# Kernel optimization log

Measured on AMD Instinct MI355X. Metric: run time of the kernel, lower is better.

The kernel has to match this reference:

```python
import jax, jax.numpy as jnp
import numpy as np

EMBED = 1024
HEADS = 16
HEAD_DIM = EMBED // HEADS

def setup_inputs() -> dict:
    key = jax.random.key(0)
    ks = jax.random.split(key, 12)
    N, L, E = 4, 2048, EMBED
    s = 1.0 / np.sqrt(E)
    return {
        "values": jax.random.normal(ks[0], (N, L, E), jnp.float32),
        "keys": jax.random.normal(ks[1], (N, L, E), jnp.float32),
        "query": jax.random.normal(ks[2], (N, L, E), jnp.float32),
        "mask": jnp.ones((N, 1, 1, L), jnp.int32),
        "Wv": jax.random.normal(ks[3], (E, E), jnp.float32) * s,
        "bv": jnp.zeros((E,), jnp.float32),
        "Wk": jax.random.normal(ks[4], (E, E), jnp.float32) * s,
        "bk": jnp.zeros((E,), jnp.float32),
        "Wq": jax.random.normal(ks[5], (E, E), jnp.float32) * s,
        "bq": jnp.zeros((E,), jnp.float32),
        "Wo": jax.random.normal(ks[6], (E, E), jnp.float32) * s,
        "bo": jnp.zeros((E,), jnp.float32),
    }

def reference(values, keys, query, mask, Wv, bv, Wk, bk, Wq, bq, Wo, bo):
    N, L, E = values.shape
    H, D = HEADS, HEAD_DIM
    v = (values @ Wv + bv).reshape(N, L, H, D)
    k = (keys @ Wk + bk).reshape(N, L, H, D)
    q = (query @ Wq + bq).reshape(N, L, H, D)
    # energy: [N, H, Lq, Lk]
    energy = jnp.einsum('nqhd,nkhd->nhqk', q, k)
    energy = jnp.where(mask == 0, jnp.float32(-1e20), energy)
    attn = jax.nn.softmax(energy / np.sqrt(D), axis=3)
    out = jnp.einsum('nhqk,nkhd->nqhd', attn, v).reshape(N, L, E)
    return out @ Wo + bo
```

## Files before the change

kernel.cpp:

```cpp
#include <hip/hip_runtime.h>
#include <hip/hip_bf16.h>


#define N_B 4
#define L_S 2048
#define E_D 1024
#define H_N 16
#define D_H 64

typedef __attribute__((ext_vector_type(8))) short short8;
typedef __attribute__((ext_vector_type(8))) unsigned short ushort8;
typedef __attribute__((ext_vector_type(4))) unsigned short ushort4v;
typedef __attribute__((ext_vector_type(4))) float f32x4;

#define EXP2F(x) __builtin_amdgcn_exp2f(x)

__device__ __forceinline__ unsigned short f2b(float f) {
    unsigned int u = __builtin_bit_cast(unsigned int, f);
    u += 0x7fffu + ((u >> 16) & 1u);
    return (unsigned short)(u >> 16);
}

__device__ __forceinline__ void gload16(const void* g, void* l) {
    __builtin_amdgcn_global_load_lds(
        (const __attribute__((address_space(1))) void*)g,
        (__attribute__((address_space(3))) void*)l, 16, 0, 0);
}

__global__ __launch_bounds__(256) void cvt3_kernel(const float* __restrict__ v,
                                                   const float* __restrict__ k,
                                                   const float* __restrict__ q,
                                                   unsigned short* __restrict__ out) {
    int z = blockIdx.y;
    const float* in = (z == 0) ? v : ((z == 1) ? k : q);
    unsigned short* o = out + (size_t)z * (8u << 20);
    size_t i = (size_t)blockIdx.x * 256 + threadIdx.x;
    const float* p = in + i * 8;
    ushort8 ov;
#pragma unroll
    for (int j = 0; j < 8; j++) ov[j] = f2b(p[j]);
    *(ushort8*)(o + i * 8) = ov;
}

__global__ __launch_bounds__(256) void wtrans4_kernel(const float* __restrict__ W0,
                                                      const float* __restrict__ W1,
                                                      const float* __restrict__ W2,
                                                      const float* __restrict__ W3,
                                                      unsigned short* __restrict__ WtBase) {
    __shared__ float t[64][65];
    int z = blockIdx.z;
    const float* W = (z == 0) ? W0 : ((z == 1) ? W1 : ((z == 2) ? W2 : W3));
    unsigned short* Wt = WtBase + (size_t)z * (1u << 20);
    int bx = blockIdx.x, by = blockIdx.y;
    int tx = threadIdx.x;
    int r0 = tx >> 4;
    int c4 = (tx & 15) << 2;
#pragma unroll
    for (int rr = 0; rr < 64; rr += 16) {
        const float* src = W + (size_t)(by * 64 + rr + r0) * E_D + bx * 64 + c4;
        float4 v = *(const float4*)src;
        t[rr + r0][c4 + 0] = v.x; t[rr + r0][c4 + 1] = v.y;
        t[rr + r0][c4 + 2] = v.z; t[rr + r0][c4 + 3] = v.w;
    }
    __syncthreads();
#pragma unroll
    for (int rr = 0; rr < 64; rr += 16) {
        int nrow = bx * 64 + rr + r0;
        ushort4v o;
#pragma unroll
        for (int j = 0; j < 4; j++) o[j] = f2b(t[c4 + j][rr + r0]);
        *(ushort4v*)(Wt + (size_t)nrow * E_D + by * 64 + c4) = o;
    }
}

template <int OUTMODE>
__device__ __forceinline__ void gemm_body(
    const unsigned short* __restrict__ A, const unsigned short* __restrict__ Bt,
    const float* __restrict__ bias, void* __restrict__ C,
    int K, int Nc, float scale,
    unsigned short* As, unsigned short* Bs, int n0, int m0) {
    int lane = threadIdx.x & 63, wave = threadIdx.x >> 6;
    int wr = (wave >> 1) * 64, wc = (wave & 1) * 64;
    f32x4 acc[4][4] = {};
    int nk = K >> 6;
    for (int kt = 0; kt < nk; ++kt) {
#pragma unroll
        for (int i = 0; i < 4; i++) {
            int c = (i * 4 + wave) * 64 + lane;
            int row = c >> 3;
            int csw = (c & 7) ^ (row & 7);
            gload16(A + (size_t)(m0 + row) * K + kt * 64 + csw * 8,
                    As + (size_t)(i * 4 + wave) * 512);
            gload16(Bt + (size_t)(n0 + row) * K + kt * 64 + csw * 8,
                    Bs + (size_t)(i * 4 + wave) * 512);
        }
        __syncthreads();
#pragma unroll
        for (int ks = 0; ks < 2; ++ks) {
            short8 a[4], b[4];
#pragma unroll
            for (int mi = 0; mi < 4; mi++) {
                int row = wr + mi * 16 + (lane & 15);
                int ch = (ks * 4 + (lane >> 4)) ^ (row & 7);
                a[mi] = *(const short8*)(As + row * 64 + ch * 8);
            }
#pragma unroll
            for (int ni = 0; ni < 4; ni++) {
                int col = wc + ni * 16 + (lane & 15);
                int ch = (ks * 4 + (lane >> 4)) ^ (col & 7);
                b[ni] = *(const short8*)(Bs + col * 64 + ch * 8);
            }
#pragma unroll
            for (int mi = 0; mi < 4; mi++)
#pragma unroll
                for (int ni = 0; ni < 4; ni++)
                    acc[mi][ni] = __builtin_amdgcn_mfma_f32_16x16x32_bf16(
                        a[mi], b[ni], acc[mi][ni], 0, 0, 0);
        }
        __syncthreads();
    }
    if (OUTMODE == 2) {
        int g = lane >> 4, c = lane & 15;
        unsigned short* tb = As + wave * 4096;
#pragma unroll
        for (int ni = 0; ni < 4; ni++) {
            int cl = ni * 16 + c;
            float bb = bias[n0 + wc + cl];
#pragma unroll
            for (int mi = 0; mi < 4; mi++) {
#pragma unroll
                for (int r = 0; r < 4; r++) {
                    int rl = mi * 16 + g * 4 + r;
                    tb[rl * 64 + (((cl >> 3) ^ (rl & 7)) << 3) + (cl & 7)] =
                        f2b((acc[mi][ni][r] + bb) * scale);
                }
            }
        }
        int mrow = m0 + wr;
        int n = mrow >> 11;
        int l0 = mrow & 2047;
        int h = (n0 + wc) >> 6;
        unsigned short* vt = (unsigned short*)C;
#pragma unroll
        for (int i = 0; i < 8; i++) {
            int d = i * 8 + (lane >> 3);
            int lc = (lane & 7) * 8;
            ushort8 ov;
#pragma unroll
            for (int j = 0; j < 8; j++) {
                int rl = lc + j;
                ov[j] = tb[rl * 64 + (((d >> 3) ^ (rl & 7)) << 3) + (d & 7)];
            }
            *(ushort8*)(vt + (size_t)((n * H_N + h) * D_H + d) * L_S + l0 + lc) = ov;
        }
        return;
    }
#pragma unroll
    for (int ni = 0; ni < 4; ni++) {
        int col = n0 + wc + ni * 16 + (lane & 15);
        float bb = bias[col];
#pragma unroll
        for (int mi = 0; mi < 4; mi++) {
            int rbase = m0 + wr + mi * 16 + (lane >> 4) * 4;
#pragma unroll
            for (int r = 0; r < 4; r++) {
                float v = (acc[mi][ni][r] + bb) * scale;
                if (OUTMODE == 1)
                    ((float*)C)[(size_t)(rbase + r) * Nc + col] = v;
                else
                    ((unsigned short*)C)[(size_t)(rbase + r) * Nc + col] = f2b(v);
            }
        }
    }
}

template <int OUTMODE>
__global__ __launch_bounds__(256, 2) void gemm_kernel(
    const unsigned short* __restrict__ A, const unsigned short* __restrict__ Bt,
    const float* __restrict__ bias, void* __restrict__ C,
    int M, int K, int Nc, float scale) {
    __shared__ unsigned short SMEM[2][128 * 64];
    gemm_body<OUTMODE>(A, Bt, bias, C, K, Nc, scale, SMEM[0], SMEM[1],
                       blockIdx.x * 128, blockIdx.y * 128);
}

__global__ __launch_bounds__(256, 2) void gemm3_kernel(
    const unsigned short* __restrict__ Abase, const unsigned short* __restrict__ Wtbase,
    const float* __restrict__ bv, const float* __restrict__ bk, const float* __restrict__ bq,
    unsigned short* __restrict__ vT, unsigned short* __restrict__ kbf,
    unsigned short* __restrict__ qbf, float qscale) {
    __shared__ unsigned short SMEM[2][128 * 64];
    int z = blockIdx.z;
    const unsigned short* A  = Abase + (size_t)z * (8u << 20);
    const unsigned short* Bt = Wtbase + (size_t)z * (1u << 20);
    int n0 = blockIdx.x * 128, m0 = blockIdx.y * 128;
    if (z == 0) {
        gemm_body<2>(A, Bt, bv, vT, E_D, E_D, 1.0f, SMEM[0], SMEM[1], n0, m0);
    } else if (z == 1) {
        gemm_body<0>(A, Bt, bk, kbf, E_D, E_D, 1.0f, SMEM[0], SMEM[1], n0, m0);
    } else {
        gemm_body<0>(A, Bt, bq, qbf, E_D, E_D, qscale, SMEM[0], SMEM[1], n0, m0);
    }
}

__global__ __launch_bounds__(512, 4) void attn_kernel(
    const unsigned short* __restrict__ qb, const unsigned short* __restrict__ kb,
    const unsigned short* __restrict__ vt, const int* __restrict__ mask,
    unsigned short* __restrict__ aout) {
    __shared__ unsigned short Ks[2][64 * 64];
    __shared__ unsigned short Vs[2][64 * 64];
    __shared__ unsigned short Ps[8][32 * 64];
    __shared__ alignas(8) unsigned char okb[256];
    int lane = threadIdx.x & 63, wave = threadIdx.x >> 6;
    int g = lane >> 4, c = lane & 15;
    const float SHIFT = 20.0f;

    int bid = blockIdx.x;
    int xcd = bid & 7, idx = bid >> 3;
    int grp = xcd * 8 + (idx >> 3);
    int q0 = (idx & 7) * 256;
    int h = grp & 15;
    int n = grp >> 4;

    const unsigned short* qptr  = qb + (size_t)n * L_S * E_D + h * 64;
    const unsigned short* kbase = kb + (size_t)n * L_S * E_D + h * 64;
    const unsigned short* vbase = vt + (size_t)(n * H_N + h) * D_H * L_S;
    const int* mbase = mask + n * L_S;

    if (threadIdx.x < 256) {
        int t8 = threadIdx.x * 8;
        int4 ma = *(const int4*)(mbase + t8);
        int4 mb = *(const int4*)(mbase + t8 + 4);
        int ok = (ma.x != 0) & (ma.y != 0) & (ma.z != 0) & (ma.w != 0) &
                 (mb.x != 0) & (mb.y != 0) & (mb.z != 0) & (mb.w != 0);
        okb[threadIdx.x] = (unsigned char)ok;
    }
    unsigned short* Qs = &Ps[0][0];
#pragma unroll
    for (int i = 0; i < 4; i++) {
        int ci = i * 8 + wave;
        int cc = ci * 64 + lane;
        int row = cc >> 3, csw = (cc & 7) ^ (row & 7);
        gload16(qptr + (size_t)(q0 + row) * E_D + csw * 8, Qs + (size_t)ci * 512);
    }
    {
        int cc = wave * 64 + lane;
        int row = cc >> 3, csw = (cc & 7) ^ (row & 7);
        gload16(kbase + (size_t)row * E_D + csw * 8, Ks[0] + wave * 512);
        gload16(vbase + (size_t)row * L_S + csw * 8, Vs[0] + wave * 512);
    }
    __syncthreads();

    short8 qf[2][2];
#pragma unroll
    for (int m = 0; m < 2; m++)
#pragma unroll
        for (int kd = 0; kd < 2; kd++) {
            int row = wave * 32 + m * 16 + c;
            int ch = (kd * 4 + g) ^ (row & 7);
            qf[m][kd] = *(const short8*)(Qs + row * 64 + ch * 8);
        }

    f32x4 o[2][4] = {};
    float lrun[2] = {0.f, 0.f};
    unsigned short* pw = &Ps[wave][0];

    const int NT = L_S / 64;
    for (int kt = 0; kt < NT; ++kt) {
        int cur = kt & 1;
        if (kt + 1 < NT) {
            int cc = wave * 64 + lane;
            int row = cc >> 3, csw = (cc & 7) ^ (row & 7);
            gload16(kbase + (size_t)((kt + 1) * 64 + row) * E_D + csw * 8,
                    Ks[cur ^ 1] + wave * 512);
            gload16(vbase + (size_t)row * L_S + (kt + 1) * 64 + csw * 8,
                    Vs[cur ^ 1] + wave * 512);
            asm volatile("s_waitcnt vmcnt(2)" ::: "memory");
        } else {
            asm volatile("s_waitcnt vmcnt(0)" ::: "memory");
        }
        __builtin_amdgcn_s_barrier();
        __builtin_amdgcn_sched_barrier(0);

        const unsigned short* KsC = Ks[cur];
        const unsigned short* VsC = Vs[cur];

        f32x4 sT[2][4] = {};
        __builtin_amdgcn_s_setprio(1);
#pragma unroll
        for (int kd = 0; kd < 2; kd++)
#pragma unroll
            for (int kg = 0; kg < 4; kg++) {
                int krow = kg * 16 + c;
                int ch = (kd * 4 + g) ^ (krow & 7);
                short8 kf = *(const short8*)(KsC + krow * 64 + ch * 8);
                sT[0][kg] = __builtin_amdgcn_mfma_f32_16x16x32_bf16(kf, qf[0][kd], sT[0][kg], 0, 0, 0);
                sT[1][kg] = __builtin_amdgcn_mfma_f32_16x16x32_bf16(kf, qf[1][kd], sT[1][kg], 0, 0, 0);
            }
        __builtin_amdgcn_s_setprio(0);

        uint2 fl = *(const uint2*)&okb[kt * 8];
        bool dense = ((fl.x & fl.y) == 0x01010101u);
        if (!dense) {
#pragma unroll
            for (int kg = 0; kg < 4; kg++) {
                int4 mv = *(const int4*)(mbase + kt * 64 + kg * 16 + g * 4);
                float m0 = mv.x ? 0.f : -1e30f;
                float m1 = mv.y ? 0.f : -1e30f;
                float m2 = mv.z ? 0.f : -1e30f;
                float m3 = mv.w ? 0.f : -1e30f;
                sT[0][kg][0] += m0; sT[1][kg][0] += m0;
                sT[0][kg][1] += m1; sT[1][kg][1] += m1;
                sT[0][kg][2] += m2; sT[1][kg][2] += m2;
                sT[0][kg][3] += m3; sT[1][kg][3] += m3;
            }
        }
#pragma unroll
        for (int m = 0; m < 2; m++) {
            float ps = 0.f;
            int prow = m * 16 + c;
#pragma unroll
            for (int kg = 0; kg < 4; kg++) {
                float p0 = EXP2F(sT[m][kg][0] - SHIFT);
                float p1 = EXP2F(sT[m][kg][1] - SHIFT);
                float p2 = EXP2F(sT[m][kg][2] - SHIFT);
                float p3 = EXP2F(sT[m][kg][3] - SHIFT);
                ps += (p0 + p1) + (p2 + p3);
                unsigned int w0, w1;
                asm("v_cvt_pk_bf16_f32 %0, %1, %2" : "=v"(w0) : "v"(p0), "v"(p1));
                asm("v_cvt_pk_bf16_f32 %0, %1, %2" : "=v"(w1) : "v"(p2), "v"(p3));
                int c16 = kg * 2 + (g >> 1);
                int off = prow * 64 + ((c16 ^ (prow & 7)) << 3) + ((g & 1) << 2);
                uint2 wv; wv.x = w0; wv.y = w1;
                *(uint2*)(pw + off) = wv;
            }
            ps += __shfl_xor(ps, 16);
            ps += __shfl_xor(ps, 32);
            lrun[m] += ps;
        }
        __builtin_amdgcn_s_setprio(1);
#pragma unroll
        for (int kk = 0; kk < 2; kk++) {
            short8 pb[2];
#pragma unroll
            for (int m = 0; m < 2; m++) {
                int prow = m * 16 + c;
                int ch = (kk * 4 + g) ^ (prow & 7);
                pb[m] = *(const short8*)(pw + prow * 64 + ch * 8);
            }
#pragma unroll
            for (int dg = 0; dg < 4; dg++) {
                int drow = dg * 16 + c;
                int ch = (kk * 4 + g) ^ (drow & 7);
                short8 vb = *(const short8*)(VsC + drow * 64 + ch * 8);
                o[0][dg] = __builtin_amdgcn_mfma_f32_16x16x32_bf16(vb, pb[0], o[0][dg], 0, 0, 0);
                o[1][dg] = __builtin_amdgcn_mfma_f32_16x16x32_bf16(vb, pb[1], o[1][dg], 0, 0, 0);
            }
        }
        __builtin_amdgcn_s_setprio(0);
        asm volatile("s_waitcnt lgkmcnt(0)" ::: "memory");
        __builtin_amdgcn_s_barrier();
    }
#pragma unroll
    for (int m = 0; m < 2; m++) {
        float inv = 1.f / lrun[m];
        int row = q0 + wave * 32 + m * 16 + c;
#pragma unroll
        for (int dg = 0; dg < 4; dg++) {
            ushort4v ov;
#pragma unroll
            for (int r = 0; r < 4; r++) ov[r] = f2b(o[m][dg][r] * inv);
            *(ushort4v*)(aout + (size_t)(n * L_S + row) * E_D + h * 64 + dg * 16 + g * 4) = ov;
        }
    }
}

extern "C" void kernel_launch(void* const* d_in, const int* in_sizes, int n_in,
                              void* d_out, int out_size, void* d_ws, size_t ws_size,
                              hipStream_t stream) {
    const float* values = (const float*)d_in[0];
    const float* keys   = (const float*)d_in[1];
    const float* query  = (const float*)d_in[2];
    const int*   mask   = (const int*)d_in[3];
    const float* Wv = (const float*)d_in[4];  const float* bv = (const float*)d_in[5];
    const float* Wk = (const float*)d_in[6];  const float* bk = (const float*)d_in[7];
    const float* Wq = (const float*)d_in[8];  const float* bq = (const float*)d_in[9];
    const float* Wo = (const float*)d_in[10]; const float* bo = (const float*)d_in[11];
    float* out = (float*)d_out;
    char* ws = (char*)d_ws;
    const size_t MB = 1ull << 20;
    unsigned short* xv  = (unsigned short*)(ws + 0 * MB);
    unsigned short* wtv = (unsigned short*)(ws + 48 * MB);
    unsigned short* wto = (unsigned short*)(ws + 54 * MB);
    unsigned short* vT  = (unsigned short*)(ws + 56 * MB);
    unsigned short* kbf = (unsigned short*)(ws + 72 * MB);
    unsigned short* qbf = (unsigned short*)(ws + 88 * MB);
    unsigned short* aob = (unsigned short*)(ws + 16 * MB);

    const float QS = 0.125f * 1.4426950408889634f;

    cvt3_kernel<<<dim3(4096, 3), 256, 0, stream>>>(values, keys, query, xv);
    wtrans4_kernel<<<dim3(16, 16, 4), 256, 0, stream>>>(Wv, Wk, Wq, Wo, wtv);
    gemm3_kernel<<<dim3(E_D / 128, (N_B * L_S) / 128, 3), 256, 0, stream>>>(
        xv, wtv, bv, bk, bq, vT, kbf, qbf, QS);
    attn_kernel<<<dim3(512), 512, 0, stream>>>(qbf, kbf, vT, mask, aob);
    gemm_kernel<1><<<dim3(E_D / 128, (N_B * L_S) / 128), 256, 0, stream>>>(
        aob, wto, bo, out, N_B * L_S, E_D, E_D, 1.0f);
}
```

Before: 212.1 us.

## Switch attention to 32x32x16 MFMA and keep P in registers

Rewrites the attention kernel's inner loop to use 32x32x16 bf16 MFMA tiles instead of 16x16x32. The probability tile is now built in registers with a cross-half-wave shuffle rather than written to and read back from per-wave LDS. This removes the Ps shared buffer, which shrinks LDS use and could allow higher occupancy, and it cuts LDS traffic. In exchange it adds lane shuffles, and the output stores become scalar 2-byte writes instead of vectorized ones.

```diff
diff --git a/kernel.cpp b/kernel.cpp
--- a/kernel.cpp
+++ b/kernel.cpp
@@ -12,6 +12,8 @@
 typedef __attribute__((ext_vector_type(8))) unsigned short ushort8;
 typedef __attribute__((ext_vector_type(4))) unsigned short ushort4v;
 typedef __attribute__((ext_vector_type(4))) float f32x4;
+typedef __attribute__((ext_vector_type(16))) float f32x16;
+typedef __attribute__((ext_vector_type(4))) unsigned int uint4v;
 
 #define EXP2F(x) __builtin_amdgcn_exp2f(x)
 
@@ -25,6 +27,12 @@
     __builtin_amdgcn_global_load_lds(
         (const __attribute__((address_space(1))) void*)g,
         (__attribute__((address_space(3))) void*)l, 16, 0, 0);
+}
+
+__device__ __forceinline__ unsigned int cvtpk(float a, float b) {
+    unsigned int w;
+    asm("v_cvt_pk_bf16_f32 %0, %1, %2" : "=v"(w) : "v"(a), "v"(b));
+    return w;
 }
 
 __global__ __launch_bounds__(256) void cvt3_kernel(const float* __restrict__ v,
@@ -207,24 +215,22 @@
     const unsigned short* __restrict__ qb, const unsigned short* __restrict__ kb,
     const unsigned short* __restrict__ vt, const int* __restrict__ mask,
     unsigned short* __restrict__ aout) {
-    __shared__ unsigned short Ks[2][64 * 64];
-    __shared__ unsigned short Vs[2][64 * 64];
-    __shared__ unsigned short Ps[8][32 * 64];
+    __shared__ unsigned short KV[4][64 * 64];
     __shared__ alignas(8) unsigned char okb[256];
     int lane = threadIdx.x & 63, wave = threadIdx.x >> 6;
-    int g = lane >> 4, c = lane & 15;
+    int qc = lane & 31, hl = lane >> 5;
     const float SHIFT = 20.0f;
 
     int bid = blockIdx.x;
     int xcd = bid & 7, idx = bid >> 3;
     int grp = xcd * 8 + (idx >> 3);
     int q0 = (idx & 7) * 256;
-    int h = grp & 15;
+    int hd = grp & 15;
     int n = grp >> 4;
 
-    const unsigned short* qptr  = qb + (size_t)n * L_S * E_D + h * 64;
-    const unsigned short* kbase = kb + (size_t)n * L_S * E_D + h * 64;
-    const unsigned short* vbase = vt + (size_t)(n * H_N + h) * D_H * L_S;
+    const unsigned short* qptr  = qb + (size_t)n * L_S * E_D + hd * 64;
+    const unsigned short* kbase = kb + (size_t)n * L_S * E_D + hd * 64;
+    const unsigned short* vbase = vt + (size_t)(n * H_N + hd) * D_H * L_S;
     const int* mbase = mask + n * L_S;
 
     if (threadIdx.x < 256) {
@@ -235,7 +241,7 @@
                  (mb.x != 0) & (mb.y != 0) & (mb.z != 0) & (mb.w != 0);
         okb[threadIdx.x] = (unsigned char)ok;
     }
-    unsigned short* Qs = &Ps[0][0];
+    unsigned short* Qs = &KV[0][0];
 #pragma unroll
     for (int i = 0; i < 4; i++) {
         int ci = i * 8 + wave;
@@ -243,27 +249,25 @@
         int row = cc >> 3, csw = (cc & 7) ^ (row & 7);
         gload16(qptr + (size_t)(q0 + row) * E_D + csw * 8, Qs + (size_t)ci * 512);
     }
+    __syncthreads();
+    short8 qf[4];
+#pragma unroll
+    for (int dk = 0; dk < 4; dk++) {
+        int row = wave * 32 + qc;
+        int ch = (dk * 2 + hl) ^ (row & 7);
+        qf[dk] = *(const short8*)(Qs + row * 64 + ch * 8);
+    }
+    asm volatile("s_waitcnt lgkmcnt(0)" ::: "memory");
+    __syncthreads();
     {
         int cc = wave * 64 + lane;
         int row = cc >> 3, csw = (cc & 7) ^ (row & 7);
-        gload16(kbase + (size_t)row * E_D + csw * 8, Ks[0] + wave * 512);
-        gload16(vbase + (size_t)row * L_S + csw * 8, Vs[0] + wave * 512);
-    }
-    __syncthreads();
-
-    short8 qf[2][2];
-#pragma unroll
-    for (int m = 0; m < 2; m++)
-#pragma unroll
-        for (int kd = 0; kd < 2; kd++) {
-            int row = wave * 32 + m * 16 + c;
-            int ch = (kd * 4 + g) ^ (row & 7);
-            qf[m][kd] = *(const short8*)(Qs + row * 64 + ch * 8);
-        }
-
-    f32x4 o[2][4] = {};
-    float lrun[2] = {0.f, 0.f};
-    unsigned short* pw = &Ps[wave][0];
+        gload16(kbase + (size_t)row * E_D + csw * 8, KV[0] + wave * 512);
+        gload16(vbase + (size_t)row * L_S + csw * 8, KV[2] + wave * 512);
+    }
+
+    f32x16 o[2] = {};
+    float lrun = 0.f;
 
     const int NT = L_S / 64;
     for (int kt = 0; kt < NT; ++kt) {
@@ -272,9 +276,9 @@
             int cc = wave * 64 + lane;
             int row = cc >> 3, csw = (cc & 7) ^ (row & 7);
             gload16(kbase + (size_t)((kt + 1) * 64 + row) * E_D + csw * 8,
-                    Ks[cur ^ 1] + wave * 512);
+                    KV[cur ^ 1] + wave * 512);
             gload16(vbase + (size_t)row * L_S + (kt + 1) * 64 + csw * 8,
-                    Vs[cur ^ 1] + wave * 512);
+                    KV[2 + (cur ^ 1)] + wave * 512);
             asm volatile("s_waitcnt vmcnt(2)" ::: "memory");
         } else {
             asm volatile("s_waitcnt vmcnt(0)" ::: "memory");
@@ -282,96 +286,82 @@
         __builtin_amdgcn_s_barrier();
         __builtin_amdgcn_sched_barrier(0);
 
-        const unsigned short* KsC = Ks[cur];
-        const unsigned short* VsC = Vs[cur];
-
-        f32x4 sT[2][4] = {};
+        const unsigned short* KsC = KV[cur];
+        const unsigned short* VsC = KV[2 + cur];
+
+        f32x16 sT0 = {}, sT1 = {};
         __builtin_amdgcn_s_setprio(1);
 #pragma unroll
-        for (int kd = 0; kd < 2; kd++)
-#pragma unroll
-            for (int kg = 0; kg < 4; kg++) {
-                int krow = kg * 16 + c;
-                int ch = (kd * 4 + g) ^ (krow & 7);
-                short8 kf = *(const short8*)(KsC + krow * 64 + ch * 8);
-                sT[0][kg] = __builtin_amdgcn_mfma_f32_16x16x32_bf16(kf, qf[0][kd], sT[0][kg], 0, 0, 0);
-                sT[1][kg] = __builtin_amdgcn_mfma_f32_16x16x32_bf16(kf, qf[1][kd], sT[1][kg], 0, 0, 0);
-            }
+        for (int dk = 0; dk < 4; dk++) {
+            int kr0 = qc, kr1 = 32 + qc;
+            int ch0 = (dk * 2 + hl) ^ (kr0 & 7);
+            int ch1 = (dk * 2 + hl) ^ (kr1 & 7);
+            short8 kf0 = *(const short8*)(KsC + kr0 * 64 + ch0 * 8);
+            short8 kf1 = *(const short8*)(KsC + kr1 * 64 + ch1 * 8);
+            sT0 = __builtin_amdgcn_mfma_f32_32x32x16_bf16(kf0, qf[dk], sT0, 0, 0, 0);
+            sT1 = __builtin_amdgcn_mfma_f32_32x32x16_bf16(kf1, qf[dk], sT1, 0, 0, 0);
+        }
         __builtin_amdgcn_s_setprio(0);
 
         uint2 fl = *(const uint2*)&okb[kt * 8];
         bool dense = ((fl.x & fl.y) == 0x01010101u);
         if (!dense) {
 #pragma unroll
-            for (int kg = 0; kg < 4; kg++) {
-                int4 mv = *(const int4*)(mbase + kt * 64 + kg * 16 + g * 4);
-                float m0 = mv.x ? 0.f : -1e30f;
-                float m1 = mv.y ? 0.f : -1e30f;
-                float m2 = mv.z ? 0.f : -1e30f;
-                float m3 = mv.w ? 0.f : -1e30f;
-                sT[0][kg][0] += m0; sT[1][kg][0] += m0;
-                sT[0][kg][1] += m1; sT[1][kg][1] += m1;
-                sT[0][kg][2] += m2; sT[1][kg][2] += m2;
-                sT[0][kg][3] += m3; sT[1][kg][3] += m3;
-            }
-        }
-#pragma unroll
-        for (int m = 0; m < 2; m++) {
-            float ps = 0.f;
-            int prow = m * 16 + c;
-#pragma unroll
-            for (int kg = 0; kg < 4; kg++) {
-                float p0 = EXP2F(sT[m][kg][0] - SHIFT);
-                float p1 = EXP2F(sT[m][kg][1] - SHIFT);
-                float p2 = EXP2F(sT[m][kg][2] - SHIFT);
-                float p3 = EXP2F(sT[m][kg][3] - SHIFT);
-                ps += (p0 + p1) + (p2 + p3);
-                unsigned int w0, w1;
-                asm("v_cvt_pk_bf16_f32 %0, %1, %2" : "=v"(w0) : "v"(p0), "v"(p1));
-                asm("v_cvt_pk_bf16_f32 %0, %1, %2" : "=v"(w1) : "v"(p2), "v"(p3));
-                int c16 = kg * 2 + (g >> 1);
-                int off = prow * 64 + ((c16 ^ (prow & 7)) << 3) + ((g & 1) << 2);
-                uint2 wv; wv.x = w0; wv.y = w1;
-                *(uint2*)(pw + off) = wv;
-            }
-            ps += __shfl_xor(ps, 16);
-            ps += __shfl_xor(ps, 32);
-            lrun[m] += ps;
-        }
-        __builtin_amdgcn_s_setprio(1);
-#pragma unroll
-        for (int kk = 0; kk < 2; kk++) {
-            short8 pb[2];
-#pragma unroll
-            for (int m = 0; m < 2; m++) {
-                int prow = m * 16 + c;
-                int ch = (kk * 4 + g) ^ (prow & 7);
-                pb[m] = *(const short8*)(pw + prow * 64 + ch * 8);
-            }
-#pragma unroll
-            for (int dg = 0; dg < 4; dg++) {
-                int drow = dg * 16 + c;
-                int ch = (kk * 4 + g) ^ (drow & 7);
-                short8 vb = *(const short8*)(VsC + drow * 64 + ch * 8);
-                o[0][dg] = __builtin_amdgcn_mfma_f32_16x16x32_bf16(vb, pb[0], o[0][dg], 0, 0, 0);
-                o[1][dg] = __builtin_amdgcn_mfma_f32_16x16x32_bf16(vb, pb[1], o[1][dg], 0, 0, 0);
-            }
-        }
-        __builtin_amdgcn_s_setprio(0);
+            for (int reg = 0; reg < 16; reg++) {
+                int crow = (reg & 3) + 8 * (reg >> 2) + 4 * hl;
+                int key = kt * 64 + crow;
+                sT0[reg] += mbase[key] ? 0.f : -1e30f;
+                sT1[reg] += mbase[key + 32] ? 0.f : -1e30f;
+            }
+        }
+        float ps = 0.f;
+#pragma unroll
+        for (int kg = 0; kg < 2; kg++) {
+            const f32x16& sS = (kg == 0) ? sT0 : sT1;
+            float p[16];
+#pragma unroll
+            for (int r = 0; r < 16; r++) {
+                p[r] = EXP2F(sS[r] - SHIFT);
+                ps += p[r];
+            }
+            unsigned int w[8], ow[8];
+#pragma unroll
+            for (int a = 0; a < 8; a++) w[a] = cvtpk(p[2 * a], p[2 * a + 1]);
+#pragma unroll
+            for (int a = 0; a < 8; a++) ow[a] = __shfl_xor(w[a], 32);
+            uint4v u0, u1;
+            u0[0] = hl ? ow[2] : w[0];  u0[1] = hl ? ow[3] : w[1];
+            u0[2] = hl ? w[2]  : ow[0]; u0[3] = hl ? w[3]  : ow[1];
+            u1[0] = hl ? ow[6] : w[4];  u1[1] = hl ? ow[7] : w[5];
+            u1[2] = hl ? w[6]  : ow[4]; u1[3] = hl ? w[7]  : ow[5];
+            short8 pa0 = __builtin_bit_cast(short8, u0);
+            short8 pa1 = __builtin_bit_cast(short8, u1);
+            __builtin_amdgcn_s_setprio(1);
+#pragma unroll
+            for (int dg = 0; dg < 2; dg++) {
+                int vr = dg * 32 + qc;
+                int c0 = (kg * 4 + 0 + hl) ^ (vr & 7);
+                int c1 = (kg * 4 + 2 + hl) ^ (vr & 7);
+                short8 vb0 = *(const short8*)(VsC + vr * 64 + c0 * 8);
+                short8 vb1 = *(const short8*)(VsC + vr * 64 + c1 * 8);
+                o[dg] = __builtin_amdgcn_mfma_f32_32x32x16_bf16(pa0, vb0, o[dg], 0, 0, 0);
+                o[dg] = __builtin_amdgcn_mfma_f32_32x32x16_bf16(pa1, vb1, o[dg], 0, 0, 0);
+            }
+            __builtin_amdgcn_s_setprio(0);
+        }
+        ps += __shfl_xor(ps, 32);
+        lrun += ps;
+
         asm volatile("s_waitcnt lgkmcnt(0)" ::: "memory");
         __builtin_amdgcn_s_barrier();
     }
 #pragma unroll
-    for (int m = 0; m < 2; m++) {
-        float inv = 1.f / lrun[m];
-        int row = q0 + wave * 32 + m * 16 + c;
-#pragma unroll
-        for (int dg = 0; dg < 4; dg++) {
-            ushort4v ov;
-#pragma unroll
-            for (int r = 0; r < 4; r++) ov[r] = f2b(o[m][dg][r] * inv);
-            *(ushort4v*)(aout + (size_t)(n * L_S + row) * E_D + h * 64 + dg * 16 + g * 4) = ov;
-        }
+    for (int reg = 0; reg < 16; reg++) {
+        int crow = (reg & 3) + 8 * (reg >> 2) + 4 * hl;
+        float iv = 1.f / __shfl(lrun, crow);
+        size_t rb = (size_t)(n * L_S + q0 + wave * 32 + crow) * E_D + hd * 64 + qc;
+        aout[rb]      = f2b(o[0][reg] * iv);
+        aout[rb + 32] = f2b(o[1][reg] * iv);
     }
 }
 
```

Measured after the change: 214.3 us. Within noise of the previous version (+1.0%).
